# Performance work log

Hardware: AMD Instinct MI355X
Metric: run time of the kernel (lower is better)

The kernel has to match this reference:

```python
import math
import jax, jax.numpy as jnp
import numpy as np

H = 16  # head_count

def setup_inputs() -> dict:
    key = jax.random.key(0)
    ks = jax.random.split(key, 7)
    B, S, D = 2, 2048, 1024
    query = jax.random.normal(ks[0], (B, S, D), dtype=jnp.float32)
    # mask: True = masked position (matches masked_fill_ semantics)
    mask = jax.random.randint(ks[1], (B, S, S), 0, 2) > 0
    scale = 1.0 / math.sqrt(D)  # xavier-ish init scale
    Wq = jax.random.normal(ks[2], (D, D), dtype=jnp.float32) * scale
    Wk = jax.random.normal(ks[3], (D, D), dtype=jnp.float32) * scale
    Wv = jax.random.normal(ks[4], (D, D), dtype=jnp.float32) * scale
    Wo = jax.random.normal(ks[5], (D, D), dtype=jnp.float32) * scale
    bo = jnp.zeros((D,), dtype=jnp.float32)
    return {"query": query, "mask": mask, "Wq": Wq, "Wk": Wk, "Wv": Wv, "Wo": Wo, "bo": bo}


def reference(query, mask, Wq, Wk, Wv, Wo, bo):
    B, S, D = query.shape
    dh = D // H

    def split_heads(x):  # [B,S,D] -> [B,H,S,dh]
        return x.reshape(B, S, H, dh).transpose(0, 2, 1, 3)

    # torch nn.Linear computes x @ W.T (bias-free for q/k/v)
    q = split_heads(query @ Wq.T) * (1.0 / math.sqrt(dh))
    k = split_heads(query @ Wk.T)
    v = split_heads(query @ Wv.T)

    scores = jnp.einsum('bhqd,bhkd->bhqk', q, k)           # [B,H,S,S]
    scores = jnp.where(mask[:, None, :, :], jnp.float32(-1e18), scores)
    weights = jax.nn.softmax(scores, axis=-1)               # dropout=0 -> identity
    ctx = jnp.einsum('bhqk,bhkd->bhqd', weights, v)         # [B,H,S,dh]
    ctx = ctx.transpose(0, 2, 1, 3).reshape(B, S, D)        # combine heads
    return ctx @ Wo.T + bo
```

## Files before the change

### kernel.cpp

```cpp
#include <hip/hip_runtime.h>

#define S_LEN 2048
#define D_MODEL 1024
#define NH 16
#define DH 64

typedef __bf16 bf16x8 __attribute__((ext_vector_type(8)));
typedef __bf16 bf16x4 __attribute__((ext_vector_type(4)));
typedef float f32x4 __attribute__((ext_vector_type(4)));

__device__ __forceinline__ unsigned short f2bf(float f) {
  unsigned int x = __float_as_uint(f);
  x += 0x7fffu + ((x >> 16) & 1u);
  return (unsigned short)(x >> 16);
}

__device__ __forceinline__ bf16x4 cvt4(f32x4 v) {
  return __builtin_convertvector(v, bf16x4);
}

__device__ __forceinline__ float exp2raw(float x) {
#if __has_builtin(__builtin_amdgcn_exp2f)
  return __builtin_amdgcn_exp2f(x);
#else
  return exp2f(x);
#endif
}

__device__ __forceinline__ f32x4 mfma16(bf16x8 a, bf16x8 b, f32x4 c) {
  return __builtin_amdgcn_mfma_f32_16x16x32_bf16(a, b, c, 0, 0, 0);
}

__device__ __forceinline__ void gl2lds(const unsigned short* g, unsigned short* l) {
  __builtin_amdgcn_global_load_lds(
      (__attribute__((address_space(1))) void*)g,
      (__attribute__((address_space(3))) void*)l, 16, 0, 0);
}

__global__ __launch_bounds__(256) void convert_kernel(
    const float* __restrict__ q, const float* __restrict__ wq,
    const float* __restrict__ wk, const float* __restrict__ wv,
    const float* __restrict__ wo, unsigned short* __restrict__ qbf,
    unsigned short* __restrict__ wbf) {
  const long t = (long)blockIdx.x * 256 + threadIdx.x;
  const float* src;
  unsigned short* dst;
  long e;
  if (t < 524288) { src = q; dst = qbf; e = t * 8; }
  else {
    long u = t - 524288;
    int wi = (int)(u >> 17);
    e = (u & 131071) * 8;
    src = wi == 0 ? wq : wi == 1 ? wk : wi == 2 ? wv : wo;
    dst = wbf + (long)wi * 1048576;
  }
  float4 a = *(const float4*)(src + e);
  float4 b = *(const float4*)(src + e + 4);
  ushort4 p0 = {f2bf(a.x), f2bf(a.y), f2bf(a.z), f2bf(a.w)};
  ushort4 p1 = {f2bf(b.x), f2bf(b.y), f2bf(b.z), f2bf(b.w)};
  *(ushort4*)(dst + e) = p0;
  *(ushort4*)(dst + e + 4) = p1;
}

__global__ void pack_mask_kernel(const int* __restrict__ mask,
                                 unsigned long long* __restrict__ bits) {
  int i = blockIdx.x * 256 + threadIdx.x;
  unsigned long long bal = __ballot(mask[i] != 0);
  if ((threadIdx.x & 63) == 0) bits[i >> 6] = bal;
}

__global__ __launch_bounds__(256) void gemm_qkv(
    const unsigned short* __restrict__ A, const unsigned short* __restrict__ W3,
    unsigned short* __restrict__ qb, unsigned short* __restrict__ kb,
    unsigned short* __restrict__ vt, float qscale) {
  __shared__ unsigned short As[128 * 64];
  __shared__ unsigned short Bs[128 * 64];
  const int tid = threadIdx.x, lane = tid & 63, wid = tid >> 6;
  const int wm = wid >> 1, wn = wid & 1;
  const int quad = lane >> 4, c = lane & 15, cx = c & 7;
  const int nG = blockIdx.x * 128;
  const int wi = nG >> 10, nn0 = nG & 1023;
  const int m0 = blockIdx.y * 128;
  const unsigned short* Bsrc = W3 + (size_t)wi * 1048576;
  const int srow = lane >> 3;
  const int schk = ((lane & 7) ^ srow) * 8;
  const unsigned short* ag = A + (size_t)(m0 + wid * 32 + srow) * 1024 + schk;
  const unsigned short* bg = Bsrc + (size_t)(nn0 + wid * 32 + srow) * 1024 + schk;
  f32x4 acc[4][4] = {};
  for (int kk = 0; kk < 1024; kk += 64) {
#pragma unroll
    for (int i = 0; i < 4; ++i) {
      gl2lds(ag + (size_t)(i * 8) * 1024 + kk, &As[(wid * 32 + i * 8) * 64]);
      gl2lds(bg + (size_t)(i * 8) * 1024 + kk, &Bs[(wid * 32 + i * 8) * 64]);
    }
    __syncthreads();
#pragma unroll
    for (int kc = 0; kc < 2; ++kc) {
      bf16x8 a[4], b[4];
#pragma unroll
      for (int mt = 0; mt < 4; ++mt)
        a[mt] = *(const bf16x8*)(
            &As[(wm * 64 + mt * 16 + c) * 64 + ((kc * 4 + quad) ^ cx) * 8]);
#pragma unroll
      for (int nt = 0; nt < 4; ++nt)
        b[nt] = *(const bf16x8*)(
            &Bs[(wn * 64 + nt * 16 + c) * 64 + ((kc * 4 + quad) ^ cx) * 8]);
#pragma unroll
      for (int mt = 0; mt < 4; ++mt)
#pragma unroll
        for (int nt = 0; nt < 4; ++nt)
          acc[mt][nt] = mfma16(a[mt], b[nt], acc[mt][nt]);
    }
    __syncthreads();
  }
#pragma unroll
  for (int mt = 0; mt < 4; ++mt) {
#pragma unroll
    for (int nt = 0; nt < 4; ++nt) {
      const int mb = m0 + wm * 64 + mt * 16 + quad * 4;
      const int n = nn0 + wn * 64 + nt * 16 + c;
      const int hh = n >> 6, d = n & 63;
      const int bb = mb >> 11, ss = mb & 2047;
      if (wi == 0) {
#pragma unroll
        for (int r = 0; r < 4; ++r)
          qb[(size_t)((bb * NH + hh) * S_LEN + ss + r) * DH + d] =
              f2bf(acc[mt][nt][r] * qscale);
      } else if (wi == 1) {
#pragma unroll
        for (int r = 0; r < 4; ++r)
          kb[(size_t)((bb * NH + hh) * S_LEN + ss + r) * DH + d] =
              f2bf(acc[mt][nt][r]);
      } else {
        *(bf16x4*)(vt + (size_t)((bb * NH + hh) * DH + d) * S_LEN + ss) =
            cvt4(acc[mt][nt]);
      }
    }
  }
}

__global__ __launch_bounds__(256) void gemm_out(
    const unsigned short* __restrict__ A, const unsigned short* __restrict__ W,
    float* __restrict__ out, const float* __restrict__ bias) {
  __shared__ unsigned short As[128 * 64];
  __shared__ unsigned short Bs[64 * 64];
  const int tid = threadIdx.x, lane = tid & 63, wid = tid >> 6;
  const int wm = wid >> 1, wn = wid & 1;
  const int quad = lane >> 4, c = lane & 15, cx = c & 7;
  const int n0 = blockIdx.x * 64, m0 = blockIdx.y * 128;
  const int srow = lane >> 3;
  const int schk = ((lane & 7) ^ srow) * 8;
  const unsigned short* ag = A + (size_t)(m0 + wid * 32 + srow) * 1024 + schk;
  const unsigned short* bg = W + (size_t)(n0 + wid * 16 + srow) * 1024 + schk;
  f32x4 acc[4][2] = {};
  for (int kk = 0; kk < 1024; kk += 64) {
#pragma unroll
    for (int i = 0; i < 4; ++i)
      gl2lds(ag + (size_t)(i * 8) * 1024 + kk, &As[(wid * 32 + i * 8) * 64]);
#pragma unroll
    for (int i = 0; i < 2; ++i)
      gl2lds(bg + (size_t)(i * 8) * 1024 + kk, &Bs[(wid * 16 + i * 8) * 64]);
    __syncthreads();
#pragma unroll
    for (int kc = 0; kc < 2; ++kc) {
      bf16x8 a[4], b[2];
#pragma unroll
      for (int mt = 0; mt < 4; ++mt)
        a[mt] = *(const bf16x8*)(
            &As[(wm * 64 + mt * 16 + c) * 64 + ((kc * 4 + quad) ^ cx) * 8]);
#pragma unroll
      for (int nt = 0; nt < 2; ++nt)
        b[nt] = *(const bf16x8*)(
            &Bs[(wn * 32 + nt * 16 + c) * 64 + ((kc * 4 + quad) ^ cx) * 8]);
#pragma unroll
      for (int mt = 0; mt < 4; ++mt)
#pragma unroll
        for (int nt = 0; nt < 2; ++nt)
          acc[mt][nt] = mfma16(a[mt], b[nt], acc[mt][nt]);
    }
    __syncthreads();
  }
#pragma unroll
  for (int mt = 0; mt < 4; ++mt) {
#pragma unroll
    for (int nt = 0; nt < 2; ++nt) {
      const int mb = m0 + wm * 64 + mt * 16 + quad * 4;
      const int n = n0 + wn * 32 + nt * 16 + c;
      const float bv = bias[n];
#pragma unroll
      for (int r = 0; r < 4; ++r)
        out[(size_t)(mb + r) * D_MODEL + n] = acc[mt][nt][r] + bv;
    }
  }
}

__global__ __launch_bounds__(256, 4) void attn_kernel(
    const unsigned short* __restrict__ qb, const unsigned short* __restrict__ kb,
    const unsigned short* __restrict__ vt,
    const unsigned long long* __restrict__ mbits,
    unsigned short* __restrict__ ctx) {
  const int h = blockIdx.x, qt = blockIdx.y, b = blockIdx.z;
  const int bh = b * NH + h;
  const int tid = threadIdx.x, lane = tid & 63, wid = tid >> 6;
  const int quad = lane >> 4, c = lane & 15, cx = c & 7;
  const int qw = wid & 1, kh = wid >> 1;
  const int q0 = qt * 64;
  __shared__ __align__(16) unsigned short KV[4][4096];

  const int qA = q0 + qw * 32 + c;
  const unsigned short* qpA = qb + (size_t)(bh * S_LEN + qA) * DH;
  bf16x8 bq[2][2];
  bq[0][0] = *(const bf16x8*)(qpA + quad * 8);
  bq[0][1] = *(const bf16x8*)(qpA + 32 + quad * 8);
  bq[1][0] = *(const bf16x8*)(qpA + 16 * DH + quad * 8);
  bq[1][1] = *(const bf16x8*)(qpA + 16 * DH + 32 + quad * 8);

  f32x4 o[2][4] = {};
  float lacc[2] = {0.f, 0.f};
  const unsigned long long* mq[2];
  mq[0] = mbits + (size_t)(b * S_LEN + qA) * 32 + kh * 16;
  mq[1] = mq[0] + 16 * 32;

  const int srow = lane >> 3, schk = ((lane & 7) ^ srow) * 8;
  const unsigned short* Ksh = KV[kh];
  const unsigned short* Vsh = KV[2 + kh];
  unsigned short* Pw = &KV[0][0] + wid * 1152;

  const unsigned short* gK =
      kb + (size_t)(bh * S_LEN + (wid & 1) * 1024 + srow) * DH + schk;
  const unsigned short* gV =
      vt + (size_t)(bh * DH + srow) * S_LEN + (wid - 2) * 1024 + schk;

  for (int kt = 0; kt < 1024; kt += 64) {
    if (wid < 2) {
#pragma unroll
      for (int i = 0; i < 8; ++i)
        gl2lds(gK + (size_t)(kt + i * 8) * DH, &KV[wid][i * 512]);
    } else {
#pragma unroll
      for (int i = 0; i < 8; ++i)
        gl2lds(gV + (size_t)(i * 8) * S_LEN + kt, &KV[wid][i * 512]);
    }
    __syncthreads();

    f32x4 s[2][4];
#pragma unroll
    for (int g = 0; g < 4; ++g) {
      const int rho = g * 16 + c;
      bf16x8 k0 = *(const bf16x8*)(&Ksh[rho * 64 + (quad ^ cx) * 8]);
      bf16x8 k1 = *(const bf16x8*)(&Ksh[rho * 64 + ((4 + quad) ^ cx) * 8]);
      f32x4 z = {};
      z = mfma16(k0, bq[0][0], z);
      z = mfma16(k1, bq[0][1], z);
      s[0][g] = z;
      f32x4 y = {};
      y = mfma16(k0, bq[1][0], y);
      y = mfma16(k1, bq[1][1], y);
      s[1][g] = y;
    }
    __syncthreads();

    const int mi = kt >> 6;
    bf16x8 bp[2][2];
#pragma unroll
    for (int sub = 0; sub < 2; ++sub) {
      const unsigned long long w64 = mq[sub][mi];
      const unsigned int wlo = (unsigned int)w64;
      const unsigned int whi = (unsigned int)(w64 >> 32);
      float lp = 0.f;
#pragma unroll
      for (int g = 0; g < 4; ++g) {
        const unsigned int bits =
            ((g & 2) ? whi : wlo) >> ((g & 1) * 16 + quad * 4);
        f32x4 p;
#pragma unroll
        for (int r = 0; r < 4; ++r) {
          const float e = exp2raw(s[sub][g][r]);
          p[r] = ((bits >> r) & 1u) ? 0.f : e;
          lp += p[r];
        }
        *(bf16x4*)(&Pw[c * 72 + g * 16 + quad * 4]) = cvt4(p);
      }
      lacc[sub] += lp;
      bp[sub][0] = *(const bf16x8*)(&Pw[c * 72 + quad * 8]);
      bp[sub][1] = *(const bf16x8*)(&Pw[c * 72 + 32 + quad * 8]);
    }

#pragma unroll
    for (int ks = 0; ks < 2; ++ks) {
#pragma unroll
      for (int nt = 0; nt < 4; ++nt) {
        bf16x8 av = *(const bf16x8*)(
            &Vsh[(nt * 16 + c) * 64 + ((ks * 4 + quad) ^ cx) * 8]);
        o[0][nt] = mfma16(av, bp[0][ks], o[0][nt]);
        o[1][nt] = mfma16(av, bp[1][ks], o[1][nt]);
      }
    }
    __syncthreads();
  }

#pragma unroll
  for (int sub = 0; sub < 2; ++sub) {
    lacc[sub] += __shfl_xor(lacc[sub], 16, 64);
    lacc[sub] += __shfl_xor(lacc[sub], 32, 64);
  }

  float* mrg = (float*)&KV[0][0];
  float* ml = mrg + 4 * 16 * 68;
  if (kh == 1) {
#pragma unroll
    for (int sub = 0; sub < 2; ++sub) {
      float* mo = mrg + (qw * 2 + sub) * 1088;
#pragma unroll
      for (int nt = 0; nt < 4; ++nt)
        *(f32x4*)(mo + c * 68 + nt * 16 + quad * 4) = o[sub][nt];
      if (quad == 0) ml[(qw * 2 + sub) * 16 + c] = lacc[sub];
    }
  }
  __syncthreads();
  if (kh == 0) {
#pragma unroll
    for (int sub = 0; sub < 2; ++sub) {
      const int pp = qw * 2 + sub;
      const float inv = 1.0f / (lacc[sub] + ml[pp * 16 + c]);
      const int q = q0 + qw * 32 + sub * 16 + c;
      const float* mo = mrg + pp * 1088;
#pragma unroll
      for (int nt = 0; nt < 4; ++nt) {
        f32x4 ob = *(const f32x4*)(mo + c * 68 + nt * 16 + quad * 4);
        f32x4 rr = (o[sub][nt] + ob) * inv;
        *(bf16x4*)(ctx + (size_t)(b * S_LEN + q) * D_MODEL + h * DH + nt * 16 +
                   quad * 4) = cvt4(rr);
      }
    }
  }
}

extern "C" void kernel_launch(void* const* d_in, const int* in_sizes, int n_in,
                              void* d_out, int out_size, void* d_ws, size_t ws_size,
                              hipStream_t stream) {
  const float* query = (const float*)d_in[0];
  const int* mask = (const int*)d_in[1];
  const float* Wq = (const float*)d_in[2];
  const float* Wk = (const float*)d_in[3];
  const float* Wv = (const float*)d_in[4];
  const float* Wo = (const float*)d_in[5];
  const float* bo = (const float*)d_in[6];
  float* out = (float*)d_out;

  char* ws = (char*)d_ws;
  const size_t MB = 1024 * 1024;
  unsigned short* qbf = (unsigned short*)(ws);
  unsigned short* wbf = (unsigned short*)(ws + 8 * MB);
  unsigned short* qb = (unsigned short*)(ws + 16 * MB);
  unsigned short* kb = (unsigned short*)(ws + 24 * MB);
  unsigned short* vt = (unsigned short*)(ws + 32 * MB);
  unsigned long long* mb = (unsigned long long*)(ws + 40 * MB);
  unsigned short* ctx = qbf;

  convert_kernel<<<4096, 256, 0, stream>>>(query, Wq, Wk, Wv, Wo, qbf, wbf);
  pack_mask_kernel<<<2 * S_LEN * S_LEN / 256, 256, 0, stream>>>(mask, mb);

  gemm_qkv<<<dim3(3072 / 128, 4096 / 128), 256, 0, stream>>>(
      qbf, wbf, qb, kb, vt, 0.18033688f);

  attn_kernel<<<dim3(NH, S_LEN / 64, 2), 256, 0, stream>>>(qb, kb, vt, mb, ctx);

  gemm_out<<<dim3(1024 / 64, 4096 / 128), 256, 0, stream>>>(
      ctx, wbf + 3 * 1048576, out, bo);
}
```

Baseline: 231.2 us.

## Merge prep kernels and restructure projection GEMMs to stage only weights in LDS

Fuses the mask-packing and fp32-to-bf16 conversion kernels into one launch. Both projection GEMMs now use 256x64 tiles. A padded 64x512 weight slab is staged in LDS across two K halves, while A fragments are read straight from global memory into registers. The aim is fewer launches and fewer barriers per K-loop and larger per-block weight reuse. The cost is uncoalesced, uncached-in-LDS global reads of A, more registers, and fewer blocks for gemm_out.

```diff
diff --git a/kernel.cpp b/kernel.cpp
--- a/kernel.cpp
+++ b/kernel.cpp
@@ -4,6 +4,7 @@
 #define D_MODEL 1024
 #define NH 16
 #define DH 64
+#define WP 520
 
 typedef __bf16 bf16x8 __attribute__((ext_vector_type(8)));
 typedef __bf16 bf16x4 __attribute__((ext_vector_type(4)));
@@ -37,90 +38,87 @@
       (__attribute__((address_space(3))) void*)l, 16, 0, 0);
 }
 
-__global__ __launch_bounds__(256) void convert_kernel(
+__global__ __launch_bounds__(256) void prep_kernel(
     const float* __restrict__ q, const float* __restrict__ wq,
     const float* __restrict__ wk, const float* __restrict__ wv,
-    const float* __restrict__ wo, unsigned short* __restrict__ qbf,
-    unsigned short* __restrict__ wbf) {
-  const long t = (long)blockIdx.x * 256 + threadIdx.x;
-  const float* src;
-  unsigned short* dst;
-  long e;
-  if (t < 524288) { src = q; dst = qbf; e = t * 8; }
-  else {
-    long u = t - 524288;
-    int wi = (int)(u >> 17);
-    e = (u & 131071) * 8;
-    src = wi == 0 ? wq : wi == 1 ? wk : wi == 2 ? wv : wo;
-    dst = wbf + (long)wi * 1048576;
-  }
-  float4 a = *(const float4*)(src + e);
-  float4 b = *(const float4*)(src + e + 4);
-  ushort4 p0 = {f2bf(a.x), f2bf(a.y), f2bf(a.z), f2bf(a.w)};
-  ushort4 p1 = {f2bf(b.x), f2bf(b.y), f2bf(b.z), f2bf(b.w)};
-  *(ushort4*)(dst + e) = p0;
-  *(ushort4*)(dst + e + 4) = p1;
-}
-
-__global__ void pack_mask_kernel(const int* __restrict__ mask,
-                                 unsigned long long* __restrict__ bits) {
-  int i = blockIdx.x * 256 + threadIdx.x;
-  unsigned long long bal = __ballot(mask[i] != 0);
-  if ((threadIdx.x & 63) == 0) bits[i >> 6] = bal;
-}
-
-__global__ __launch_bounds__(256) void gemm_qkv(
+    const float* __restrict__ wo, const int* __restrict__ mask,
+    unsigned short* __restrict__ qbf, unsigned short* __restrict__ wbf,
+    unsigned long long* __restrict__ bits) {
+  const int bx = blockIdx.x;
+  if (bx < 32768) {
+    int i = bx * 256 + threadIdx.x;
+    unsigned long long bal = __ballot(mask[i] != 0);
+    if ((threadIdx.x & 63) == 0) bits[i >> 6] = bal;
+  } else {
+    const long t = (long)(bx - 32768) * 256 + threadIdx.x;
+    const float* src;
+    unsigned short* dst;
+    long e;
+    if (t < 524288) { src = q; dst = qbf; e = t * 8; }
+    else {
+      long u = t - 524288;
+      int wi = (int)(u >> 17);
+      e = (u & 131071) * 8;
+      src = wi == 0 ? wq : wi == 1 ? wk : wi == 2 ? wv : wo;
+      dst = wbf + (long)wi * 1048576;
+    }
+    float4 a = *(const float4*)(src + e);
+    float4 b = *(const float4*)(src + e + 4);
+    ushort4 p0 = {f2bf(a.x), f2bf(a.y), f2bf(a.z), f2bf(a.w)};
+    ushort4 p1 = {f2bf(b.x), f2bf(b.y), f2bf(b.z), f2bf(b.w)};
+    *(ushort4*)(dst + e) = p0;
+    *(ushort4*)(dst + e + 4) = p1;
+  }
+}
+
+__global__ __launch_bounds__(256, 2) void gemm_qkv(
     const unsigned short* __restrict__ A, const unsigned short* __restrict__ W3,
     unsigned short* __restrict__ qb, unsigned short* __restrict__ kb,
     unsigned short* __restrict__ vt, float qscale) {
-  __shared__ unsigned short As[128 * 64];
-  __shared__ unsigned short Bs[128 * 64];
+  __shared__ __align__(16) unsigned short Ws[64 * WP];
   const int tid = threadIdx.x, lane = tid & 63, wid = tid >> 6;
-  const int wm = wid >> 1, wn = wid & 1;
-  const int quad = lane >> 4, c = lane & 15, cx = c & 7;
-  const int nG = blockIdx.x * 128;
+  const int quad = lane >> 4, c = lane & 15;
+  const int nG = blockIdx.x * 64;
   const int wi = nG >> 10, nn0 = nG & 1023;
-  const int m0 = blockIdx.y * 128;
-  const unsigned short* Bsrc = W3 + (size_t)wi * 1048576;
-  const int srow = lane >> 3;
-  const int schk = ((lane & 7) ^ srow) * 8;
-  const unsigned short* ag = A + (size_t)(m0 + wid * 32 + srow) * 1024 + schk;
-  const unsigned short* bg = Bsrc + (size_t)(nn0 + wid * 32 + srow) * 1024 + schk;
+  const int hh = nn0 >> 6;
+  const int m0 = blockIdx.y * 256;
+  const unsigned short* Wsrc =
+      W3 + (size_t)wi * 1048576 + (size_t)nn0 * 1024 + lane * 8;
   f32x4 acc[4][4] = {};
-  for (int kk = 0; kk < 1024; kk += 64) {
-#pragma unroll
-    for (int i = 0; i < 4; ++i) {
-      gl2lds(ag + (size_t)(i * 8) * 1024 + kk, &As[(wid * 32 + i * 8) * 64]);
-      gl2lds(bg + (size_t)(i * 8) * 1024 + kk, &Bs[(wid * 32 + i * 8) * 64]);
-    }
-    __syncthreads();
-#pragma unroll
-    for (int kc = 0; kc < 2; ++kc) {
+#pragma unroll
+  for (int p = 0; p < 2; ++p) {
+#pragma unroll
+    for (int i = 0; i < 16; ++i) {
+      const int row = wid * 16 + i;
+      gl2lds(Wsrc + (size_t)row * 1024 + p * 512, &Ws[row * WP]);
+    }
+    __syncthreads();
+#pragma unroll 4
+    for (int kc = 0; kc < 16; ++kc) {
       bf16x8 a[4], b[4];
 #pragma unroll
       for (int mt = 0; mt < 4; ++mt)
-        a[mt] = *(const bf16x8*)(
-            &As[(wm * 64 + mt * 16 + c) * 64 + ((kc * 4 + quad) ^ cx) * 8]);
+        a[mt] = *(const bf16x8*)(A +
+                                 (size_t)(m0 + wid * 64 + mt * 16 + c) * 1024 +
+                                 p * 512 + kc * 32 + quad * 8);
 #pragma unroll
       for (int nt = 0; nt < 4; ++nt)
-        b[nt] = *(const bf16x8*)(
-            &Bs[(wn * 64 + nt * 16 + c) * 64 + ((kc * 4 + quad) ^ cx) * 8]);
+        b[nt] = *(const bf16x8*)(&Ws[(nt * 16 + c) * WP + (kc * 4 + quad) * 8]);
 #pragma unroll
       for (int mt = 0; mt < 4; ++mt)
 #pragma unroll
         for (int nt = 0; nt < 4; ++nt)
           acc[mt][nt] = mfma16(a[mt], b[nt], acc[mt][nt]);
     }
-    __syncthreads();
-  }
+    if (p == 0) __syncthreads();
+  }
+  const int bb = m0 >> 11;
 #pragma unroll
   for (int mt = 0; mt < 4; ++mt) {
 #pragma unroll
     for (int nt = 0; nt < 4; ++nt) {
-      const int mb = m0 + wm * 64 + mt * 16 + quad * 4;
-      const int n = nn0 + wn * 64 + nt * 16 + c;
-      const int hh = n >> 6, d = n & 63;
-      const int bb = mb >> 11, ss = mb & 2047;
+      const int ss = (m0 & 2047) + wid * 64 + mt * 16 + quad * 4;
+      const int d = nt * 16 + c;
       if (wi == 0) {
 #pragma unroll
         for (int r = 0; r < 4; ++r)
@@ -139,53 +137,48 @@
   }
 }
 
-__global__ __launch_bounds__(256) void gemm_out(
+__global__ __launch_bounds__(256, 2) void gemm_out(
     const unsigned short* __restrict__ A, const unsigned short* __restrict__ W,
     float* __restrict__ out, const float* __restrict__ bias) {
-  __shared__ unsigned short As[128 * 64];
-  __shared__ unsigned short Bs[64 * 64];
+  __shared__ __align__(16) unsigned short Ws[64 * WP];
   const int tid = threadIdx.x, lane = tid & 63, wid = tid >> 6;
-  const int wm = wid >> 1, wn = wid & 1;
-  const int quad = lane >> 4, c = lane & 15, cx = c & 7;
-  const int n0 = blockIdx.x * 64, m0 = blockIdx.y * 128;
-  const int srow = lane >> 3;
-  const int schk = ((lane & 7) ^ srow) * 8;
-  const unsigned short* ag = A + (size_t)(m0 + wid * 32 + srow) * 1024 + schk;
-  const unsigned short* bg = W + (size_t)(n0 + wid * 16 + srow) * 1024 + schk;
-  f32x4 acc[4][2] = {};
-  for (int kk = 0; kk < 1024; kk += 64) {
-#pragma unroll
-    for (int i = 0; i < 4; ++i)
-      gl2lds(ag + (size_t)(i * 8) * 1024 + kk, &As[(wid * 32 + i * 8) * 64]);
-#pragma unroll
-    for (int i = 0; i < 2; ++i)
-      gl2lds(bg + (size_t)(i * 8) * 1024 + kk, &Bs[(wid * 16 + i * 8) * 64]);
-    __syncthreads();
-#pragma unroll
-    for (int kc = 0; kc < 2; ++kc) {
-      bf16x8 a[4], b[2];
+  const int quad = lane >> 4, c = lane & 15;
+  const int n0 = blockIdx.x * 64, m0 = blockIdx.y * 256;
+  const unsigned short* Wsrc = W + (size_t)n0 * 1024 + lane * 8;
+  f32x4 acc[4][4] = {};
+#pragma unroll
+  for (int p = 0; p < 2; ++p) {
+#pragma unroll
+    for (int i = 0; i < 16; ++i) {
+      const int row = wid * 16 + i;
+      gl2lds(Wsrc + (size_t)row * 1024 + p * 512, &Ws[row * WP]);
+    }
+    __syncthreads();
+#pragma unroll 4
+    for (int kc = 0; kc < 16; ++kc) {
+      bf16x8 a[4], b[4];
 #pragma unroll
       for (int mt = 0; mt < 4; ++mt)
-        a[mt] = *(const bf16x8*)(
-            &As[(wm * 64 + mt * 16 + c) * 64 + ((kc * 4 + quad) ^ cx) * 8]);
-#pragma unroll
-      for (int nt = 0; nt < 2; ++nt)
-        b[nt] = *(const bf16x8*)(
-            &Bs[(wn * 32 + nt * 16 + c) * 64 + ((kc * 4 + quad) ^ cx) * 8]);
+        a[mt] = *(const bf16x8*)(A +
+                                 (size_t)(m0 + wid * 64 + mt * 16 + c) * 1024 +
+                                 p * 512 + kc * 32 + quad * 8);
+#pragma unroll
+      for (int nt = 0; nt < 4; ++nt)
+        b[nt] = *(const bf16x8*)(&Ws[(nt * 16 + c) * WP + (kc * 4 + quad) * 8]);
 #pragma unroll
       for (int mt = 0; mt < 4; ++mt)
 #pragma unroll
-        for (int nt = 0; nt < 2; ++nt)
+        for (int nt = 0; nt < 4; ++nt)
           acc[mt][nt] = mfma16(a[mt], b[nt], acc[mt][nt]);
     }
-    __syncthreads();
+    if (p == 0) __syncthreads();
   }
 #pragma unroll
   for (int mt = 0; mt < 4; ++mt) {
 #pragma unroll
-    for (int nt = 0; nt < 2; ++nt) {
-      const int mb = m0 + wm * 64 + mt * 16 + quad * 4;
-      const int n = n0 + wn * 32 + nt * 16 + c;
+    for (int nt = 0; nt < 4; ++nt) {
+      const int mb = m0 + wid * 64 + mt * 16 + quad * 4;
+      const int n = n0 + nt * 16 + c;
       const float bv = bias[n];
 #pragma unroll
       for (int r = 0; r < 4; ++r)
@@ -358,14 +351,14 @@
   unsigned long long* mb = (unsigned long long*)(ws + 40 * MB);
   unsigned short* ctx = qbf;
 
-  convert_kernel<<<4096, 256, 0, stream>>>(query, Wq, Wk, Wv, Wo, qbf, wbf);
-  pack_mask_kernel<<<2 * S_LEN * S_LEN / 256, 256, 0, stream>>>(mask, mb);
-
-  gemm_qkv<<<dim3(3072 / 128, 4096 / 128), 256, 0, stream>>>(
+  prep_kernel<<<32768 + 4096, 256, 0, stream>>>(query, Wq, Wk, Wv, Wo, mask,
+                                                qbf, wbf, mb);
+
+  gemm_qkv<<<dim3(3072 / 64, 4096 / 256), 256, 0, stream>>>(
       qbf, wbf, qb, kb, vt, 0.18033688f);
 
   attn_kernel<<<dim3(NH, S_LEN / 64, 2), 256, 0, stream>>>(qb, kb, vt, mb, ctx);
 
-  gemm_out<<<dim3(1024 / 64, 4096 / 128), 256, 0, stream>>>(
+  gemm_out<<<dim3(1024 / 64, 4096 / 256), 256, 0, stream>>>(
       ctx, wbf + 3 * 1048576, out, bo);
 }
```

Measured after the change: 268.1 us. 1.16x slower.

## Double attention query tile per block and merge prep kernels into one launch

Applied to the files above, without the earlier changes.

Each attention block now handles 128 query rows instead of 64, so every K/V tile loaded into LDS serves twice as many queries. This halves total K/V global traffic and the number of barrier-separated loads per query. Per-wave P buffers move into a separate LDS array, which drops one __syncthreads per iteration, and launch bounds are relaxed to 2 blocks per CU to fit the larger register and LDS footprint. The mask-packing and fp32-to-bf16 conversion kernels are fused into a single launch to save launch overhead, at the cost of fewer attention blocks (512) and lower occupancy.

```diff
diff --git a/kernel.cpp b/kernel.cpp
--- a/kernel.cpp
+++ b/kernel.cpp
@@ -37,36 +37,37 @@
       (__attribute__((address_space(3))) void*)l, 16, 0, 0);
 }
 
-__global__ __launch_bounds__(256) void convert_kernel(
+__global__ __launch_bounds__(256) void prep_kernel(
     const float* __restrict__ q, const float* __restrict__ wq,
     const float* __restrict__ wk, const float* __restrict__ wv,
-    const float* __restrict__ wo, unsigned short* __restrict__ qbf,
-    unsigned short* __restrict__ wbf) {
-  const long t = (long)blockIdx.x * 256 + threadIdx.x;
-  const float* src;
-  unsigned short* dst;
-  long e;
-  if (t < 524288) { src = q; dst = qbf; e = t * 8; }
-  else {
-    long u = t - 524288;
-    int wi = (int)(u >> 17);
-    e = (u & 131071) * 8;
-    src = wi == 0 ? wq : wi == 1 ? wk : wi == 2 ? wv : wo;
-    dst = wbf + (long)wi * 1048576;
-  }
-  float4 a = *(const float4*)(src + e);
-  float4 b = *(const float4*)(src + e + 4);
-  ushort4 p0 = {f2bf(a.x), f2bf(a.y), f2bf(a.z), f2bf(a.w)};
-  ushort4 p1 = {f2bf(b.x), f2bf(b.y), f2bf(b.z), f2bf(b.w)};
-  *(ushort4*)(dst + e) = p0;
-  *(ushort4*)(dst + e + 4) = p1;
-}
-
-__global__ void pack_mask_kernel(const int* __restrict__ mask,
-                                 unsigned long long* __restrict__ bits) {
-  int i = blockIdx.x * 256 + threadIdx.x;
-  unsigned long long bal = __ballot(mask[i] != 0);
-  if ((threadIdx.x & 63) == 0) bits[i >> 6] = bal;
+    const float* __restrict__ wo, const int* __restrict__ mask,
+    unsigned short* __restrict__ qbf, unsigned short* __restrict__ wbf,
+    unsigned long long* __restrict__ bits) {
+  const int bx = blockIdx.x;
+  if (bx < 32768) {
+    int i = bx * 256 + threadIdx.x;
+    unsigned long long bal = __ballot(mask[i] != 0);
+    if ((threadIdx.x & 63) == 0) bits[i >> 6] = bal;
+  } else {
+    const long t = (long)(bx - 32768) * 256 + threadIdx.x;
+    const float* src;
+    unsigned short* dst;
+    long e;
+    if (t < 524288) { src = q; dst = qbf; e = t * 8; }
+    else {
+      long u = t - 524288;
+      int wi = (int)(u >> 17);
+      e = (u & 131071) * 8;
+      src = wi == 0 ? wq : wi == 1 ? wk : wi == 2 ? wv : wo;
+      dst = wbf + (long)wi * 1048576;
+    }
+    float4 a = *(const float4*)(src + e);
+    float4 b = *(const float4*)(src + e + 4);
+    ushort4 p0 = {f2bf(a.x), f2bf(a.y), f2bf(a.z), f2bf(a.w)};
+    ushort4 p1 = {f2bf(b.x), f2bf(b.y), f2bf(b.z), f2bf(b.w)};
+    *(ushort4*)(dst + e) = p0;
+    *(ushort4*)(dst + e + 4) = p1;
+  }
 }
 
 __global__ __launch_bounds__(256) void gemm_qkv(
@@ -194,7 +195,7 @@
   }
 }
 
-__global__ __launch_bounds__(256, 4) void attn_kernel(
+__global__ __launch_bounds__(256, 2) void attn_kernel(
     const unsigned short* __restrict__ qb, const unsigned short* __restrict__ kb,
     const unsigned short* __restrict__ vt,
     const unsigned long long* __restrict__ mbits,
@@ -204,27 +205,28 @@
   const int tid = threadIdx.x, lane = tid & 63, wid = tid >> 6;
   const int quad = lane >> 4, c = lane & 15, cx = c & 7;
   const int qw = wid & 1, kh = wid >> 1;
-  const int q0 = qt * 64;
+  const int q0 = qt * 128;
   __shared__ __align__(16) unsigned short KV[4][4096];
-
-  const int qA = q0 + qw * 32 + c;
-  const unsigned short* qpA = qb + (size_t)(bh * S_LEN + qA) * DH;
-  bf16x8 bq[2][2];
-  bq[0][0] = *(const bf16x8*)(qpA + quad * 8);
-  bq[0][1] = *(const bf16x8*)(qpA + 32 + quad * 8);
-  bq[1][0] = *(const bf16x8*)(qpA + 16 * DH + quad * 8);
-  bq[1][1] = *(const bf16x8*)(qpA + 16 * DH + 32 + quad * 8);
-
-  f32x4 o[2][4] = {};
-  float lacc[2] = {0.f, 0.f};
-  const unsigned long long* mq[2];
-  mq[0] = mbits + (size_t)(b * S_LEN + qA) * 32 + kh * 16;
-  mq[1] = mq[0] + 16 * 32;
+  __shared__ __align__(16) unsigned short Pbuf[4][64 * 72];
+
+  const int qbase = q0 + qw * 64;
+  const unsigned short* qp = qb + (size_t)(bh * S_LEN + qbase + c) * DH;
+  bf16x8 bq[4][2];
+#pragma unroll
+  for (int sub = 0; sub < 4; ++sub) {
+    bq[sub][0] = *(const bf16x8*)(qp + sub * 16 * DH + quad * 8);
+    bq[sub][1] = *(const bf16x8*)(qp + sub * 16 * DH + 32 + quad * 8);
+  }
+
+  f32x4 o[4][4] = {};
+  float lacc[4] = {0.f, 0.f, 0.f, 0.f};
+  const unsigned long long* mq0 =
+      mbits + (size_t)(b * S_LEN + qbase + c) * 32 + kh * 16;
 
   const int srow = lane >> 3, schk = ((lane & 7) ^ srow) * 8;
   const unsigned short* Ksh = KV[kh];
   const unsigned short* Vsh = KV[2 + kh];
-  unsigned short* Pw = &KV[0][0] + wid * 1152;
+  unsigned short* Pw = Pbuf[wid];
 
   const unsigned short* gK =
       kb + (size_t)(bh * S_LEN + (wid & 1) * 1024 + srow) * DH + schk;
@@ -243,28 +245,26 @@
     }
     __syncthreads();
 
-    f32x4 s[2][4];
+    bf16x8 kf[8];
 #pragma unroll
     for (int g = 0; g < 4; ++g) {
       const int rho = g * 16 + c;
-      bf16x8 k0 = *(const bf16x8*)(&Ksh[rho * 64 + (quad ^ cx) * 8]);
-      bf16x8 k1 = *(const bf16x8*)(&Ksh[rho * 64 + ((4 + quad) ^ cx) * 8]);
-      f32x4 z = {};
-      z = mfma16(k0, bq[0][0], z);
-      z = mfma16(k1, bq[0][1], z);
-      s[0][g] = z;
-      f32x4 y = {};
-      y = mfma16(k0, bq[1][0], y);
-      y = mfma16(k1, bq[1][1], y);
-      s[1][g] = y;
-    }
-    __syncthreads();
+      kf[2 * g] = *(const bf16x8*)(&Ksh[rho * 64 + (quad ^ cx) * 8]);
+      kf[2 * g + 1] = *(const bf16x8*)(&Ksh[rho * 64 + ((4 + quad) ^ cx) * 8]);
+    }
 
     const int mi = kt >> 6;
-    bf16x8 bp[2][2];
-#pragma unroll
-    for (int sub = 0; sub < 2; ++sub) {
-      const unsigned long long w64 = mq[sub][mi];
+#pragma unroll
+    for (int sub = 0; sub < 4; ++sub) {
+      f32x4 s[4];
+#pragma unroll
+      for (int g = 0; g < 4; ++g) {
+        f32x4 z = {};
+        z = mfma16(kf[2 * g], bq[sub][0], z);
+        z = mfma16(kf[2 * g + 1], bq[sub][1], z);
+        s[g] = z;
+      }
+      const unsigned long long w64 = mq0[sub * 512 + mi];
       const unsigned int wlo = (unsigned int)w64;
       const unsigned int whi = (unsigned int)(w64 >> 32);
       float lp = 0.f;
@@ -275,55 +275,59 @@
         f32x4 p;
 #pragma unroll
         for (int r = 0; r < 4; ++r) {
-          const float e = exp2raw(s[sub][g][r]);
+          const float e = exp2raw(s[g][r]);
           p[r] = ((bits >> r) & 1u) ? 0.f : e;
           lp += p[r];
         }
-        *(bf16x4*)(&Pw[c * 72 + g * 16 + quad * 4]) = cvt4(p);
+        *(bf16x4*)(&Pw[(sub * 16 + c) * 72 + g * 16 + quad * 4]) = cvt4(p);
       }
       lacc[sub] += lp;
-      bp[sub][0] = *(const bf16x8*)(&Pw[c * 72 + quad * 8]);
-      bp[sub][1] = *(const bf16x8*)(&Pw[c * 72 + 32 + quad * 8]);
     }
 
 #pragma unroll
     for (int ks = 0; ks < 2; ++ks) {
+      bf16x8 bp[4];
+#pragma unroll
+      for (int sub = 0; sub < 4; ++sub)
+        bp[sub] =
+            *(const bf16x8*)(&Pw[(sub * 16 + c) * 72 + ks * 32 + quad * 8]);
 #pragma unroll
       for (int nt = 0; nt < 4; ++nt) {
         bf16x8 av = *(const bf16x8*)(
             &Vsh[(nt * 16 + c) * 64 + ((ks * 4 + quad) ^ cx) * 8]);
-        o[0][nt] = mfma16(av, bp[0][ks], o[0][nt]);
-        o[1][nt] = mfma16(av, bp[1][ks], o[1][nt]);
-      }
-    }
-    __syncthreads();
-  }
-
-#pragma unroll
-  for (int sub = 0; sub < 2; ++sub) {
+#pragma unroll
+        for (int sub = 0; sub < 4; ++sub)
+          o[sub][nt] = mfma16(av, bp[sub], o[sub][nt]);
+      }
+    }
+    __syncthreads();
+  }
+
+#pragma unroll
+  for (int sub = 0; sub < 4; ++sub) {
     lacc[sub] += __shfl_xor(lacc[sub], 16, 64);
     lacc[sub] += __shfl_xor(lacc[sub], 32, 64);
   }
 
-  float* mrg = (float*)&KV[0][0];
-  float* ml = mrg + 4 * 16 * 68;
+  float* mrg = (float*)&Pbuf[0][0];
+  float* ml = mrg + 8 * 1088;
   if (kh == 1) {
 #pragma unroll
-    for (int sub = 0; sub < 2; ++sub) {
-      float* mo = mrg + (qw * 2 + sub) * 1088;
+    for (int sub = 0; sub < 4; ++sub) {
+      float* mo = mrg + (qw * 4 + sub) * 1088;
 #pragma unroll
       for (int nt = 0; nt < 4; ++nt)
         *(f32x4*)(mo + c * 68 + nt * 16 + quad * 4) = o[sub][nt];
-      if (quad == 0) ml[(qw * 2 + sub) * 16 + c] = lacc[sub];
+      if (quad == 0) ml[(qw * 4 + sub) * 16 + c] = lacc[sub];
     }
   }
   __syncthreads();
   if (kh == 0) {
 #pragma unroll
-    for (int sub = 0; sub < 2; ++sub) {
-      const int pp = qw * 2 + sub;
+    for (int sub = 0; sub < 4; ++sub) {
+      const int pp = qw * 4 + sub;
       const float inv = 1.0f / (lacc[sub] + ml[pp * 16 + c]);
-      const int q = q0 + qw * 32 + sub * 16 + c;
+      const int q = qbase + sub * 16 + c;
       const float* mo = mrg + pp * 1088;
 #pragma unroll
       for (int nt = 0; nt < 4; ++nt) {
@@ -358,13 +362,14 @@
   unsigned long long* mb = (unsigned long long*)(ws + 40 * MB);
   unsigned short* ctx = qbf;
 
-  convert_kernel<<<4096, 256, 0, stream>>>(query, Wq, Wk, Wv, Wo, qbf, wbf);
-  pack_mask_kernel<<<2 * S_LEN * S_LEN / 256, 256, 0, stream>>>(mask, mb);
+  prep_kernel<<<32768 + 4096, 256, 0, stream>>>(query, Wq, Wk, Wv, Wo, mask,
+                                                qbf, wbf, mb);
 
   gemm_qkv<<<dim3(3072 / 128, 4096 / 128), 256, 0, stream>>>(
       qbf, wbf, qb, kb, vt, 0.18033688f);
 
-  attn_kernel<<<dim3(NH, S_LEN / 64, 2), 256, 0, stream>>>(qb, kb, vt, mb, ctx);
+  attn_kernel<<<dim3(NH, S_LEN / 128, 2), 256, 0, stream>>>(qb, kb, vt, mb,
+                                                            ctx);
 
   gemm_out<<<dim3(1024 / 64, 4096 / 128), 256, 0, stream>>>(
       ctx, wbf + 3 * 1048576, out, bo);
```

Result: faster. 224.3 us (-3.0%).
